# Kernel tuning notes

Hardware: AMD Instinct MI355X
Metric: run time of the kernel (lower is better)

Reference implementation:

```python
import jax, jax.numpy as jnp
import numpy as np

B, S, E, H = 4, 1024, 1024, 16
HD = E // H  # 64


def setup_inputs() -> dict:
    key = jax.random.key(0)
    ks = jax.random.split(key, 9)
    scale = 1.0 / np.sqrt(E)
    x = jax.random.normal(ks[0], (B, S, E), dtype=jnp.float32)
    attention_mask = jnp.ones((B, S, S), dtype=jnp.int32)
    # per-head projection weights, batched over heads: [H, E, HD]
    Wq = jax.random.normal(ks[1], (H, E, HD), dtype=jnp.float32) * scale
    Wk = jax.random.normal(ks[2], (H, E, HD), dtype=jnp.float32) * scale
    Wv = jax.random.normal(ks[3], (H, E, HD), dtype=jnp.float32) * scale
    bq = jax.random.normal(ks[4], (H, HD), dtype=jnp.float32) * scale
    bk = jax.random.normal(ks[5], (H, HD), dtype=jnp.float32) * scale
    bv = jax.random.normal(ks[6], (H, HD), dtype=jnp.float32) * scale
    # output projection, torch Linear convention: [out_features, in_features]
    Wo = jax.random.normal(ks[7], (E, E), dtype=jnp.float32) * scale
    bo = jax.random.normal(ks[8], (E,), dtype=jnp.float32) * scale
    return {"x": x, "attention_mask": attention_mask, "Wq": Wq, "bq": bq,
            "Wk": Wk, "bk": bk, "Wv": Wv, "bv": bv, "Wo": Wo, "bo": bo}


def reference(x, attention_mask, Wq, bq, Wk, bk, Wv, bv, Wo, bo):
    # batched-over-heads QKV projections: (B,S,E) x (H,E,HD) -> (B,H,S,HD)
    q = jnp.einsum('bse,hed->bhsd', x, Wq) + bq[None, :, None, :]
    k = jnp.einsum('bse,hed->bhsd', x, Wk) + bk[None, :, None, :]
    v = jnp.einsum('bse,hed->bhsd', x, Wv) + bv[None, :, None, :]
    scores = jnp.einsum('bhsd,bhtd->bhst', q, k) / jnp.sqrt(jnp.float32(HD))
    mask = attention_mask[:, None, :, :]  # (B,1,S,S) broadcast over heads
    scores = jnp.where(mask == 0, -jnp.inf, scores)
    weights = jax.nn.softmax(scores, axis=-1)
    out = jnp.einsum('bhst,bhtd->bhsd', weights, v)
    # concat heads on last dim: (B,S,H*HD) == (B,S,E)
    out = out.transpose(0, 2, 1, 3).reshape(B, S, E)
    return out @ Wo.T + bo
```

## Files before the change

### kernel.cpp

```cpp
#include <hip/hip_runtime.h>
#include <hip/hip_bf16.h>

#define NB 4
#define SEQ 1024
#define EMB 1024
#define NH 16
#define HD 64

typedef unsigned short u16;
typedef __attribute__((ext_vector_type(8))) __bf16 bf16x8;
typedef __attribute__((ext_vector_type(8))) short short8;
typedef __attribute__((ext_vector_type(4))) float floatx4;

__device__ inline u16 f2b_rn(float f) {
    union { float f; unsigned int i; } x; x.f = f;
    unsigned int r = (x.i + 0x7FFFu + ((x.i >> 16) & 1u)) >> 16;
    return (u16)r;
}
__device__ inline bf16x8 s2b(short8 v) {
    union { short8 s; bf16x8 b; } x; x.s = v; return x.b;
}

__device__ inline void gload_lds16(const void* g, void* l) {
    __builtin_amdgcn_global_load_lds(
        (const __attribute__((address_space(1))) void*)g,
        (__attribute__((address_space(3))) void*)l, 16, 0, 0);
}

__device__ inline bf16x8 ldsfrag(const u16* base, int r, int c) {
    return s2b(*(const short8*)&base[r * 64 + (c ^ ((r & 7) * 8))]);
}

__device__ inline void cvt8(const float* __restrict__ s, u16* __restrict__ d) {
    float4 a = *(const float4*)(s);
    float4 b = *(const float4*)(s + 4);
    union { u16 u[8]; int4 v; } o;
    o.u[0] = f2b_rn(a.x); o.u[1] = f2b_rn(a.y); o.u[2] = f2b_rn(a.z); o.u[3] = f2b_rn(a.w);
    o.u[4] = f2b_rn(b.x); o.u[5] = f2b_rn(b.y); o.u[6] = f2b_rn(b.z); o.u[7] = f2b_rn(b.w);
    *(int4*)(d) = o.v;
}

#define BARX do { __builtin_amdgcn_sched_barrier(0); __builtin_amdgcn_s_barrier(); __builtin_amdgcn_sched_barrier(0); } while(0)
#define VMCNT6 asm volatile("s_waitcnt vmcnt(6)" ::: "memory")
#define VMCNT5 asm volatile("s_waitcnt vmcnt(5)" ::: "memory")
#define VMCNT2 asm volatile("s_waitcnt vmcnt(2)" ::: "memory")
#define VMCNT0 asm volatile("s_waitcnt vmcnt(0)" ::: "memory")

__global__ __launch_bounds__(256) void prep(
    const float* __restrict__ x, const float* __restrict__ Wq,
    const float* __restrict__ Wk, const float* __restrict__ Wv,
    const int* __restrict__ mask,
    u16* __restrict__ xb, u16* __restrict__ Wt,
    unsigned long long* __restrict__ bits)
{
    __shared__ u16 T[64 * 80];
    int bx = blockIdx.x;
    int tid = threadIdx.x;

    if (bx < 512) {
        #pragma unroll
        for (int c = 0; c < 4; ++c) {
            int i = (bx * 4 + c) * 2048 + tid * 8;
            cvt8(x + i, xb + i);
        }
    } else if (bx < 1280) {
        int bx2 = bx - 512;
        int e0 = (bx2 & 15) * 64;
        int ph = bx2 >> 4;
        int p = ph >> 4, h = ph & 15;
        const float* W = (p == 0 ? Wq : (p == 1 ? Wk : Wv)) + h * (EMB * HD);
        #pragma unroll
        for (int c = 0; c < 2; ++c) {
            int flat = c * 2048 + tid * 8;
            int r = flat >> 6;
            int d = flat & 63;
            cvt8(W + (size_t)(e0 + r) * HD + d, &T[r * 80 + d]);
        }
        __syncthreads();
        int d = tid >> 2;
        int ec = tid & 3;
        union { u16 u[16]; int4 v[2]; } tmp;
        #pragma unroll
        for (int i = 0; i < 16; ++i) tmp.u[i] = T[(ec * 16 + i) * 80 + d];
        u16* dst = Wt + ((size_t)(p * NH + h) * HD + d) * EMB + e0 + ec * 16;
        *(int4*)(dst) = tmp.v[0];
        *(int4*)(dst + 8) = tmp.v[1];
    } else {
        int base = (bx - 1280) * 16 + (tid >> 6) * 4;
        int lane = tid & 63;
        #pragma unroll
        for (int i = 0; i < 4; ++i) {
            int gw = base + i;
            int m = mask[(size_t)gw * 64 + lane];
            unsigned long long bl = __ballot(m != 0);
            if (lane == 0) bits[gw] = bl;
        }
    }
}

__device__ __forceinline__ void rd_b(const u16* B, int wn, int ln, int quad, bf16x8 (&bfr)[4][2]) {
    #pragma unroll
    for (int nc = 0; nc < 4; ++nc) {
        bfr[nc][0] = ldsfrag(B, wn * 64 + nc * 16 + ln, quad * 8);
        bfr[nc][1] = ldsfrag(B, wn * 64 + nc * 16 + ln, 32 + quad * 8);
    }
}
__device__ __forceinline__ void rd_a(const u16* A, int wm, int mf0, int ln, int quad, bf16x8 (&a)[2][2]) {
    #pragma unroll
    for (int jj = 0; jj < 2; ++jj) {
        a[jj][0] = ldsfrag(A, wm * 128 + (mf0 + jj) * 16 + ln, quad * 8);
        a[jj][1] = ldsfrag(A, wm * 128 + (mf0 + jj) * 16 + ln, 32 + quad * 8);
    }
}
__device__ __forceinline__ void mm8(floatx4 (&acc)[8][4], const bf16x8 (&a)[2][2],
                                    const bf16x8 (&bfr)[4][2], int mf0) {
    #pragma unroll
    for (int jj = 0; jj < 2; ++jj)
        #pragma unroll
        for (int nc = 0; nc < 4; ++nc) {
            acc[mf0 + jj][nc] = __builtin_amdgcn_mfma_f32_16x16x32_bf16(a[jj][0], bfr[nc][0], acc[mf0 + jj][nc], 0, 0, 0);
            acc[mf0 + jj][nc] = __builtin_amdgcn_mfma_f32_16x16x32_bf16(a[jj][1], bfr[nc][1], acc[mf0 + jj][nc], 0, 0, 0);
        }
}

#define STG(srcb, buf, c, kt) gload_lds16((srcb) + (size_t)(c) * 65536 + (kt) * 64 + soff, (buf) + (c) * 4096 + ldst)

__global__ __launch_bounds__(512, 2) void qkv_gemm(
    const u16* __restrict__ x,
    const u16* __restrict__ Wt2,
    const float* __restrict__ bq, const float* __restrict__ bk, const float* __restrict__ bv,
    u16* __restrict__ Q, u16* __restrict__ K, u16* __restrict__ Vt)
{
    __shared__ u16 L[65536];
    u16* A0s = L;
    u16* A1s = L + 16384;
    u16* B0s = L + 32768;
    u16* B1s = L + 49152;

    int gid = blockIdx.x;
    int xcd = gid & 7;
    int j   = gid >> 3;
    int mt_ = (xcd >> 1) * 4 + (j & 3);
    int nt_ = (xcd & 1) * 6 + (j >> 2);
    int m0 = mt_ * 256;
    int n0 = nt_ * 256;

    int tid = threadIdx.x;
    int w = tid >> 6, lane = tid & 63, quad = lane >> 4, ln = lane & 15;
    int wm = w >> 2, wn = w & 3;

    const u16* Asrc = x   + (size_t)m0 * EMB;
    const u16* Bsrc = Wt2 + (size_t)n0 * EMB;

    int sr = tid >> 3;
    int sc = ((tid & 7) ^ (sr & 7)) * 8;
    size_t soff = (size_t)sr * EMB + sc;
    int ldst = w * 512;

    STG(Asrc, A0s, 0, 0); STG(Asrc, A0s, 1, 0); STG(Asrc, A0s, 2, 0); STG(Asrc, A0s, 3, 0);
    STG(Bsrc, B0s, 0, 0); STG(Bsrc, B0s, 1, 0); STG(Bsrc, B0s, 2, 0); STG(Bsrc, B0s, 3, 0);
    STG(Bsrc, B1s, 0, 1); STG(Bsrc, B1s, 1, 1); STG(Bsrc, B1s, 2, 1); STG(Bsrc, B1s, 3, 1);
    STG(Asrc, A1s, 0, 1); STG(Asrc, A1s, 2, 1);
    VMCNT6;
    BARX;

    floatx4 acc[8][4] = {};
    bf16x8 bfr[4][2];
    bf16x8 a[2][2];

    for (int i = 0; i < 8; ++i) {
        const int T = 2 * i;
        const bool st = (i < 7);
        rd_b(B0s, wn, ln, quad, bfr);
        rd_a(A0s, wm, 0, ln, quad, a);
        STG(Asrc, A1s, 1, T + 1); STG(Asrc, A1s, 3, T + 1);
        BARX;
        __builtin_amdgcn_s_setprio(1); mm8(acc, a, bfr, 0); __builtin_amdgcn_s_setprio(0);
        BARX;
        rd_a(A0s, wm, 2, ln, quad, a);
        if (st) { STG(Bsrc, B0s, 0, T + 2); STG(Bsrc, B0s, 1, T + 2); }
        BARX;
        __builtin_amdgcn_s_setprio(1); mm8(acc, a, bfr, 2); __builtin_amdgcn_s_setprio(0);
        BARX;
        rd_a(A0s, wm, 4, ln, quad, a);
        if (st) { STG(Bsrc, B0s, 2, T + 2); STG(Bsrc, B0s, 3, T + 2); }
        BARX;
        __builtin_amdgcn_s_setprio(1); mm8(acc, a, bfr, 4); __builtin_amdgcn_s_setprio(0);
        BARX;
        rd_a(A0s, wm, 6, ln, quad, a);
        if (st) { STG(Asrc, A0s, 0, T + 2); STG(Asrc, A0s, 2, T + 2); }
        BARX;
        __builtin_amdgcn_s_setprio(1); mm8(acc, a, bfr, 6); __builtin_amdgcn_s_setprio(0);
        if (st) { VMCNT6; } else { VMCNT0; }
        BARX;
        rd_b(B1s, wn, ln, quad, bfr);
        rd_a(A1s, wm, 0, ln, quad, a);
        if (st) { STG(Asrc, A0s, 1, T + 2); STG(Asrc, A0s, 3, T + 2); }
        BARX;
        __builtin_amdgcn_s_setprio(1); mm8(acc, a, bfr, 0); __builtin_amdgcn_s_setprio(0);
        BARX;
        rd_a(A1s, wm, 2, ln, quad, a);
        if (st) { STG(Bsrc, B1s, 0, T + 3); STG(Bsrc, B1s, 1, T + 3); }
        BARX;
        __builtin_amdgcn_s_setprio(1); mm8(acc, a, bfr, 2); __builtin_amdgcn_s_setprio(0);
        BARX;
        rd_a(A1s, wm, 4, ln, quad, a);
        if (st) { STG(Bsrc, B1s, 2, T + 3); STG(Bsrc, B1s, 3, T + 3); }
        BARX;
        __builtin_amdgcn_s_setprio(1); mm8(acc, a, bfr, 4); __builtin_amdgcn_s_setprio(0);
        BARX;
        rd_a(A1s, wm, 6, ln, quad, a);
        if (st) { STG(Asrc, A1s, 0, T + 3); STG(Asrc, A1s, 2, T + 3); }
        BARX;
        __builtin_amdgcn_s_setprio(1); mm8(acc, a, bfr, 6); __builtin_amdgcn_s_setprio(0);
        if (st) { VMCNT6; }
        BARX;
    }

    int nbase = n0 + wn * 64;
    int p = nbase >> 10;
    int h = (nbase >> 6) & 15;
    const float* bias = (p == 0 ? bq : (p == 1 ? bk : bv));
    if (p < 2) {
        u16* Out = (p == 0) ? Q : K;
        float qs = (p == 0) ? 0.125f * 1.44269504f : 1.0f;
        #pragma unroll
        for (int nc = 0; nc < 4; ++nc) {
            int d = nc * 16 + ln;
            float bv_ = bias[(nbase & 1023) + d];
            #pragma unroll
            for (int mf = 0; mf < 8; ++mf) {
                #pragma unroll
                for (int reg = 0; reg < 4; ++reg) {
                    int m = m0 + wm * 128 + mf * 16 + quad * 4 + reg;
                    int b_ = m >> 10, s = m & 1023;
                    Out[((size_t)(b_ * NH + h) * SEQ + s) * HD + d] = f2b_rn((acc[mf][nc][reg] + bv_) * qs);
                }
            }
        }
    } else {
        #pragma unroll
        for (int nc = 0; nc < 4; ++nc) {
            int d = nc * 16 + ln;
            float bv_ = bias[(nbase & 1023) + d];
            #pragma unroll
            for (int mf = 0; mf < 8; ++mf) {
                int m = m0 + wm * 128 + mf * 16 + quad * 4;
                int b_ = m >> 10, s = m & 1023;
                union { u16 u[4]; uint2 v; } pk;
                #pragma unroll
                for (int reg = 0; reg < 4; ++reg)
                    pk.u[reg] = f2b_rn(acc[mf][nc][reg] + bv_);
                *(uint2*)&Vt[((size_t)(b_ * NH + h) * HD + d) * SEQ + s] = pk.v;
            }
        }
    }
}

__device__ __forceinline__ void astage(const u16* __restrict__ Kb, const u16* __restrict__ Vb,
                                       u16* Kd, u16* Vd, int t0, int tid) {
    #pragma unroll
    for (int i = 0; i < 2; ++i) {
        int flat0 = i * 256 + (tid & 192);
        int flat = flat0 + (tid & 63);
        int r = flat >> 3;
        int c = ((flat & 7) ^ (r & 7)) * 8;
        gload_lds16(Kb + (size_t)(t0 + r) * HD + c, Kd + flat0 * 8);
        gload_lds16(Vb + (size_t)r * SEQ + t0 + c, Vd + flat0 * 8);
    }
}

__device__ __forceinline__ void attn_tile(
    const u16* Ksc, const u16* Vsc, u16* Ps,
    const bf16x8 (&qf)[2][2], floatx4 (&o)[2][5],
    unsigned long long bm0, unsigned long long bm1,
    int w, int ln, int quad)
{
    const int PP = 72;
    floatx4 sc[2][4] = {};
    #pragma unroll
    for (int kk = 0; kk < 2; ++kk) {
        bf16x8 kf[4];
        #pragma unroll
        for (int tb = 0; tb < 4; ++tb)
            kf[tb] = ldsfrag(Ksc, tb * 16 + ln, kk * 32 + quad * 8);
        __builtin_amdgcn_s_setprio(1);
        #pragma unroll
        for (int s = 0; s < 2; ++s)
            #pragma unroll
            for (int tb = 0; tb < 4; ++tb)
                sc[s][tb] = __builtin_amdgcn_mfma_f32_16x16x32_bf16(kf[tb], qf[s][kk], sc[s][tb], 0, 0, 0);
        __builtin_amdgcn_s_setprio(0);
    }

    #pragma unroll
    for (int s = 0; s < 2; ++s) {
        unsigned long long bm = s ? bm1 : bm0;
        if (__any(bm != ~0ull)) {
            #pragma unroll
            for (int tb = 0; tb < 4; ++tb)
                #pragma unroll
                for (int reg = 0; reg < 4; ++reg)
                    if (!((bm >> (tb * 16 + quad * 4 + reg)) & 1)) sc[s][tb][reg] = -1e30f;
        }
    }

    #pragma unroll
    for (int s = 0; s < 2; ++s) {
        int mrow = w * 32 + s * 16 + ln;
        #pragma unroll
        for (int tb = 0; tb < 4; ++tb) {
            union { float f; unsigned int i; } e0_, e1_, e2_, e3_;
            e0_.f = __builtin_amdgcn_exp2f(sc[s][tb][0]);
            e1_.f = __builtin_amdgcn_exp2f(sc[s][tb][1]);
            e2_.f = __builtin_amdgcn_exp2f(sc[s][tb][2]);
            e3_.f = __builtin_amdgcn_exp2f(sc[s][tb][3]);
            uint2 pk;
            pk.x = ((e0_.i + 0x8000u) >> 16) | ((e1_.i + 0x8000u) & 0xFFFF0000u);
            pk.y = ((e2_.i + 0x8000u) >> 16) | ((e3_.i + 0x8000u) & 0xFFFF0000u);
            *(uint2*)&Ps[mrow * PP + tb * 16 + quad * 4] = pk;
        }
    }

    #pragma unroll
    for (int kk = 0; kk < 2; ++kk) {
        bf16x8 vf[5];
        #pragma unroll
        for (int dt = 0; dt < 5; ++dt)
            vf[dt] = ldsfrag(Vsc, dt * 16 + ln, kk * 32 + quad * 8);
        #pragma unroll
        for (int s = 0; s < 2; ++s) {
            bf16x8 pf = s2b(*(const short8*)&Ps[(w * 32 + s * 16 + ln) * PP + kk * 32 + quad * 8]);
            __builtin_amdgcn_s_setprio(1);
            #pragma unroll
            for (int dt = 0; dt < 5; ++dt)
                o[s][dt] = __builtin_amdgcn_mfma_f32_16x16x32_bf16(pf, vf[dt], o[s][dt], 0, 0, 0);
            __builtin_amdgcn_s_setprio(0);
        }
    }
}

__global__ __launch_bounds__(256) void attn(
    const u16* __restrict__ Q, const u16* __restrict__ K, const u16* __restrict__ Vt,
    const unsigned long long* __restrict__ bits,
    const float* __restrict__ Wo, u16* __restrict__ Wob,
    u16* __restrict__ Aout)
{
    __shared__ u16 L[16512 + 128 * 72];
    u16* Ks0 = L;
    u16* Ks1 = L + 4096;
    u16* Vs0 = L + 8192;
    u16* Vs1 = L + 12352;
    u16* Ps  = L + 16512;

    int bid = blockIdx.x;
    int tid = threadIdx.x;

    if (bid >= 512) {
        int i = (bid - 512) * 2048 + tid * 8;
        cvt8(Wo + i, Wob + i);
        return;
    }

    int bh = bid & 63;
    int q0 = (bid >> 6) * 128;
    int b = bh >> 4, h = bh & 15;
    const u16* Qb = Q  + (size_t)bh * SEQ * HD;
    const u16* Kb = K  + (size_t)bh * SEQ * HD;
    const u16* Vb = Vt + (size_t)bh * HD * SEQ;

    int w = tid >> 6, lane = tid & 63, quad = lane >> 4, ln = lane & 15;

    if (tid < 32) {
        u16* dst = (tid < 16 ? L + 12288 : L + 16448) + (tid & 15) * 4;
        *(uint2*)dst = make_uint2(0x3F803F80u, 0x3F803F80u);
    }

    bf16x8 qf[2][2];
    #pragma unroll
    for (int s = 0; s < 2; ++s) {
        const u16* qp = Qb + (size_t)(q0 + w * 32 + s * 16 + ln) * HD + quad * 8;
        union { int4 i; bf16x8 b; } c0, c1;
        c0.i = *(const int4*)(qp);
        c1.i = *(const int4*)(qp + 32);
        qf[s][0] = c0.b; qf[s][1] = c1.b;
    }

    __syncthreads();

    astage(Kb, Vb, Ks0, Vs0, 0,  tid);
    astage(Kb, Vb, Ks1, Vs1, 64, tid);
    size_t bb0 = ((size_t)b * SEQ + q0 + w * 32 + ln) * 16;
    size_t bb1 = bb0 + 256;
    unsigned long long bmn0 = bits[bb0];
    unsigned long long bmn1 = bits[bb1];

    floatx4 o[2][5] = {};

    for (int i = 0; i < 8; ++i) {
        VMCNT6;
        BARX;
        {
            unsigned long long bc0 = bmn0, bc1 = bmn1;
            bmn0 = bits[bb0 + (2 * i + 1)];
            bmn1 = bits[bb1 + (2 * i + 1)];
            attn_tile(Ks0, Vs0, Ps, qf, o, bc0, bc1, w, ln, quad);
        }
        BARX;
        if (i < 7) astage(Kb, Vb, Ks0, Vs0, i * 128 + 128, tid);
        if (i < 7) { VMCNT6; } else { VMCNT2; }
        BARX;
        {
            unsigned long long bc0 = bmn0, bc1 = bmn1;
            if (i < 7) { bmn0 = bits[bb0 + (2 * i + 2)]; bmn1 = bits[bb1 + (2 * i + 2)]; }
            attn_tile(Ks1, Vs1, Ps, qf, o, bc0, bc1, w, ln, quad);
        }
        BARX;
        if (i < 7) astage(Kb, Vb, Ks1, Vs1, i * 128 + 192, tid);
    }

    #pragma unroll
    for (int s = 0; s < 2; ++s) {
        #pragma unroll
        for (int reg = 0; reg < 4; ++reg) {
            float l = __shfl(o[s][4][reg], lane & 48, 64);
            float inv = 1.0f / l;
            int m = q0 + w * 32 + s * 16 + quad * 4 + reg;
            #pragma unroll
            for (int dt = 0; dt < 4; ++dt)
                Aout[((size_t)b * SEQ + m) * EMB + h * HD + dt * 16 + ln] = f2b_rn(o[s][dt][reg] * inv);
        }
    }
}

#define OSTG_A(buf, kt) gload_lds16(Asrc + (size_t)(kt) * 64 + soff, (buf) + ldst)
#define OSTG_B(buf, c, kt) gload_lds16(Bsrc + (size_t)(c) * 65536 + (size_t)(kt) * 64 + soff, (buf) + (c) * 4096 + ldst)

__device__ __forceinline__ void op_tile(const u16* As, const u16* Bs,
                                        floatx4 (&acc)[4][2], int w, int ln, int quad)
{
    #pragma unroll
    for (int kk = 0; kk < 2; ++kk) {
        bf16x8 av[4], bv2[2];
        #pragma unroll
        for (int mf = 0; mf < 4; ++mf)
            av[mf] = ldsfrag(As, mf * 16 + ln, kk * 32 + quad * 8);
        #pragma unroll
        for (int nc = 0; nc < 2; ++nc)
            bv2[nc] = ldsfrag(Bs, w * 32 + nc * 16 + ln, kk * 32 + quad * 8);
        __builtin_amdgcn_s_setprio(1);
        #pragma unroll
        for (int mf = 0; mf < 4; ++mf)
            #pragma unroll
            for (int nc = 0; nc < 2; ++nc)
                acc[mf][nc] = __builtin_amdgcn_mfma_f32_16x16x32_bf16(av[mf], bv2[nc], acc[mf][nc], 0, 0, 0);
        __builtin_amdgcn_s_setprio(0);
    }
}

__global__ __launch_bounds__(512, 2) void out_proj(
    const u16* __restrict__ A,
    const u16* __restrict__ Wo,
    const float* __restrict__ bo,
    float* __restrict__ Out)
{
    __shared__ u16 L[40960];
    u16* A0s = L;
    u16* A1s = L + 4096;
    u16* B0s = L + 8192;
    u16* B1s = L + 24576;

    int gid = blockIdx.x;
    int xcd = gid & 7;
    int j   = gid >> 3;
    int m0 = (xcd * 8 + (j & 7)) * 64;
    int n0 = (j >> 3) * 256;

    int tid = threadIdx.x;
    int w = tid >> 6, lane = tid & 63, quad = lane >> 4, ln = lane & 15;

    const u16* Asrc = A  + (size_t)m0 * EMB;
    const u16* Bsrc = Wo + (size_t)n0 * EMB;
    int sr = tid >> 3;
    int sc = ((tid & 7) ^ (sr & 7)) * 8;
    size_t soff = (size_t)sr * EMB + sc;
    int ldst = w * 512;

    OSTG_A(A0s, 0); OSTG_B(B0s, 0, 0); OSTG_B(B0s, 1, 0); OSTG_B(B0s, 2, 0); OSTG_B(B0s, 3, 0);
    OSTG_A(A1s, 1); OSTG_B(B1s, 0, 1); OSTG_B(B1s, 1, 1); OSTG_B(B1s, 2, 1); OSTG_B(B1s, 3, 1);

    floatx4 acc[4][2] = {};

    for (int i = 0; i < 8; ++i) {
        VMCNT5;
        BARX;
        op_tile(A0s, B0s, acc, w, ln, quad);
        BARX;
        if (i < 7) {
            int kt = 2 * i + 2;
            OSTG_A(A0s, kt); OSTG_B(B0s, 0, kt); OSTG_B(B0s, 1, kt); OSTG_B(B0s, 2, kt); OSTG_B(B0s, 3, kt);
        }
        if (i < 7) { VMCNT5; } else { VMCNT0; }
        BARX;
        op_tile(A1s, B1s, acc, w, ln, quad);
        BARX;
        if (i < 7) {
            int kt = 2 * i + 3;
            OSTG_A(A1s, kt); OSTG_B(B1s, 0, kt); OSTG_B(B1s, 1, kt); OSTG_B(B1s, 2, kt); OSTG_B(B1s, 3, kt);
        }
    }

    #pragma unroll
    for (int nc = 0; nc < 2; ++nc) {
        int n = n0 + w * 32 + nc * 16 + ln;
        float bb = bo[n];
        #pragma unroll
        for (int mf = 0; mf < 4; ++mf) {
            #pragma unroll
            for (int reg = 0; reg < 4; ++reg) {
                int m = m0 + mf * 16 + quad * 4 + reg;
                Out[(size_t)m * EMB + n] = acc[mf][nc][reg] + bb;
            }
        }
    }
}

extern "C" void kernel_launch(void* const* d_in, const int* in_sizes, int n_in,
                              void* d_out, int out_size, void* d_ws, size_t ws_size,
                              hipStream_t stream) {
    const float* x  = (const float*)d_in[0];
    const int*   mk = (const int*)d_in[1];
    const float* Wq = (const float*)d_in[2];
    const float* bq = (const float*)d_in[3];
    const float* Wk = (const float*)d_in[4];
    const float* bk = (const float*)d_in[5];
    const float* Wv = (const float*)d_in[6];
    const float* bv = (const float*)d_in[7];
    const float* Wo = (const float*)d_in[8];
    const float* bo = (const float*)d_in[9];
    float* out = (float*)d_out;

    const size_t MB = 1u << 20;
    char* ws = (char*)d_ws;
    u16* xb  = (u16*)ws;
    u16* Wt  = (u16*)(ws + 8 * MB);
    u16* Wob = (u16*)(ws + 14 * MB);
    unsigned long long* bits = (unsigned long long*)(ws + 16 * MB);
    u16* Qw  = (u16*)(ws + 16 * MB + 512 * 1024);
    u16* Kw  = (u16*)(ws + 24 * MB + 512 * 1024);
    u16* Vtw = (u16*)(ws + 32 * MB + 512 * 1024);
    u16* Ao  = xb;

    prep<<<5376, 256, 0, stream>>>(x, Wq, Wk, Wv, mk, xb, Wt, bits);
    qkv_gemm<<<192, 512, 0, stream>>>(xb, Wt, bq, bk, bv, Qw, Kw, Vtw);
    attn<<<1024, 256, 0, stream>>>(Qw, Kw, Vtw, bits, Wo, Wob, Ao);
    out_proj<<<256, 512, 0, stream>>>(Ao, Wob, bo, out);
}
```

Before: 183.9 us.

## Shrink QKV GEMM N-tile to 192 so grid fills all 256 CUs

Changes the QKV projection GEMM tile from 256x256 to 256x192, which raises the grid from 192 to 256 blocks so every CU on the MI355X gets work. The B stage shrinks to three chunks, the staging schedule and vmcnt waits are rebalanced, and the epilogue now resolves projection and head per 16-column fragment because a 192-wide tile can straddle heads and Q/K/V. The aim is to remove the wave quantization that left CUs idle. The cost is lower arithmetic intensity per block and a more complex epilogue.

```diff
diff --git a/kernel.cpp b/kernel.cpp
--- a/kernel.cpp
+++ b/kernel.cpp
@@ -98,11 +98,11 @@
     }
 }
 
-__device__ __forceinline__ void rd_b(const u16* B, int wn, int ln, int quad, bf16x8 (&bfr)[4][2]) {
-    #pragma unroll
-    for (int nc = 0; nc < 4; ++nc) {
-        bfr[nc][0] = ldsfrag(B, wn * 64 + nc * 16 + ln, quad * 8);
-        bfr[nc][1] = ldsfrag(B, wn * 64 + nc * 16 + ln, 32 + quad * 8);
+__device__ __forceinline__ void rd_b3(const u16* B, int wn, int ln, int quad, bf16x8 (&bfr)[3][2]) {
+    #pragma unroll
+    for (int nc = 0; nc < 3; ++nc) {
+        bfr[nc][0] = ldsfrag(B, wn * 48 + nc * 16 + ln, quad * 8);
+        bfr[nc][1] = ldsfrag(B, wn * 48 + nc * 16 + ln, 32 + quad * 8);
     }
 }
 __device__ __forceinline__ void rd_a(const u16* A, int wm, int mf0, int ln, int quad, bf16x8 (&a)[2][2]) {
@@ -112,12 +112,12 @@
         a[jj][1] = ldsfrag(A, wm * 128 + (mf0 + jj) * 16 + ln, 32 + quad * 8);
     }
 }
-__device__ __forceinline__ void mm8(floatx4 (&acc)[8][4], const bf16x8 (&a)[2][2],
-                                    const bf16x8 (&bfr)[4][2], int mf0) {
+__device__ __forceinline__ void mm12(floatx4 (&acc)[8][3], const bf16x8 (&a)[2][2],
+                                     const bf16x8 (&bfr)[3][2], int mf0) {
     #pragma unroll
     for (int jj = 0; jj < 2; ++jj)
         #pragma unroll
-        for (int nc = 0; nc < 4; ++nc) {
+        for (int nc = 0; nc < 3; ++nc) {
             acc[mf0 + jj][nc] = __builtin_amdgcn_mfma_f32_16x16x32_bf16(a[jj][0], bfr[nc][0], acc[mf0 + jj][nc], 0, 0, 0);
             acc[mf0 + jj][nc] = __builtin_amdgcn_mfma_f32_16x16x32_bf16(a[jj][1], bfr[nc][1], acc[mf0 + jj][nc], 0, 0, 0);
         }
@@ -131,19 +131,19 @@
     const float* __restrict__ bq, const float* __restrict__ bk, const float* __restrict__ bv,
     u16* __restrict__ Q, u16* __restrict__ K, u16* __restrict__ Vt)
 {
-    __shared__ u16 L[65536];
+    __shared__ u16 L[57344];
     u16* A0s = L;
     u16* A1s = L + 16384;
     u16* B0s = L + 32768;
-    u16* B1s = L + 49152;
+    u16* B1s = L + 45056;
 
     int gid = blockIdx.x;
     int xcd = gid & 7;
     int j   = gid >> 3;
     int mt_ = (xcd >> 1) * 4 + (j & 3);
-    int nt_ = (xcd & 1) * 6 + (j >> 2);
+    int nt_ = (xcd & 1) * 8 + (j >> 2);
     int m0 = mt_ * 256;
-    int n0 = nt_ * 256;
+    int n0 = nt_ * 192;
 
     int tid = threadIdx.x;
     int w = tid >> 6, lane = tid & 63, quad = lane >> 4, ln = lane & 15;
@@ -158,76 +158,77 @@
     int ldst = w * 512;
 
     STG(Asrc, A0s, 0, 0); STG(Asrc, A0s, 1, 0); STG(Asrc, A0s, 2, 0); STG(Asrc, A0s, 3, 0);
-    STG(Bsrc, B0s, 0, 0); STG(Bsrc, B0s, 1, 0); STG(Bsrc, B0s, 2, 0); STG(Bsrc, B0s, 3, 0);
-    STG(Bsrc, B1s, 0, 1); STG(Bsrc, B1s, 1, 1); STG(Bsrc, B1s, 2, 1); STG(Bsrc, B1s, 3, 1);
+    STG(Bsrc, B0s, 0, 0); STG(Bsrc, B0s, 1, 0); STG(Bsrc, B0s, 2, 0);
+    STG(Bsrc, B1s, 0, 1); STG(Bsrc, B1s, 1, 1); STG(Bsrc, B1s, 2, 1);
     STG(Asrc, A1s, 0, 1); STG(Asrc, A1s, 2, 1);
-    VMCNT6;
+    VMCNT5;
     BARX;
 
-    floatx4 acc[8][4] = {};
-    bf16x8 bfr[4][2];
+    floatx4 acc[8][3] = {};
+    bf16x8 bfr[3][2];
     bf16x8 a[2][2];
 
     for (int i = 0; i < 8; ++i) {
         const int T = 2 * i;
         const bool st = (i < 7);
-        rd_b(B0s, wn, ln, quad, bfr);
+        rd_b3(B0s, wn, ln, quad, bfr);
         rd_a(A0s, wm, 0, ln, quad, a);
         STG(Asrc, A1s, 1, T + 1); STG(Asrc, A1s, 3, T + 1);
         BARX;
-        __builtin_amdgcn_s_setprio(1); mm8(acc, a, bfr, 0); __builtin_amdgcn_s_setprio(0);
+        __builtin_amdgcn_s_setprio(1); mm12(acc, a, bfr, 0); __builtin_amdgcn_s_setprio(0);
         BARX;
         rd_a(A0s, wm, 2, ln, quad, a);
         if (st) { STG(Bsrc, B0s, 0, T + 2); STG(Bsrc, B0s, 1, T + 2); }
         BARX;
-        __builtin_amdgcn_s_setprio(1); mm8(acc, a, bfr, 2); __builtin_amdgcn_s_setprio(0);
+        __builtin_amdgcn_s_setprio(1); mm12(acc, a, bfr, 2); __builtin_amdgcn_s_setprio(0);
         BARX;
         rd_a(A0s, wm, 4, ln, quad, a);
-        if (st) { STG(Bsrc, B0s, 2, T + 2); STG(Bsrc, B0s, 3, T + 2); }
-        BARX;
-        __builtin_amdgcn_s_setprio(1); mm8(acc, a, bfr, 4); __builtin_amdgcn_s_setprio(0);
+        if (st) { STG(Bsrc, B0s, 2, T + 2); STG(Asrc, A0s, 0, T + 2); }
+        BARX;
+        __builtin_amdgcn_s_setprio(1); mm12(acc, a, bfr, 4); __builtin_amdgcn_s_setprio(0);
         BARX;
         rd_a(A0s, wm, 6, ln, quad, a);
-        if (st) { STG(Asrc, A0s, 0, T + 2); STG(Asrc, A0s, 2, T + 2); }
-        BARX;
-        __builtin_amdgcn_s_setprio(1); mm8(acc, a, bfr, 6); __builtin_amdgcn_s_setprio(0);
-        if (st) { VMCNT6; } else { VMCNT0; }
-        BARX;
-        rd_b(B1s, wn, ln, quad, bfr);
+        if (st) { STG(Asrc, A0s, 2, T + 2); }
+        BARX;
+        __builtin_amdgcn_s_setprio(1); mm12(acc, a, bfr, 6); __builtin_amdgcn_s_setprio(0);
+        if (st) { VMCNT5; } else { VMCNT0; }
+        BARX;
+        rd_b3(B1s, wn, ln, quad, bfr);
         rd_a(A1s, wm, 0, ln, quad, a);
         if (st) { STG(Asrc, A0s, 1, T + 2); STG(Asrc, A0s, 3, T + 2); }
         BARX;
-        __builtin_amdgcn_s_setprio(1); mm8(acc, a, bfr, 0); __builtin_amdgcn_s_setprio(0);
+        __builtin_amdgcn_s_setprio(1); mm12(acc, a, bfr, 0); __builtin_amdgcn_s_setprio(0);
         BARX;
         rd_a(A1s, wm, 2, ln, quad, a);
         if (st) { STG(Bsrc, B1s, 0, T + 3); STG(Bsrc, B1s, 1, T + 3); }
         BARX;
-        __builtin_amdgcn_s_setprio(1); mm8(acc, a, bfr, 2); __builtin_amdgcn_s_setprio(0);
+        __builtin_amdgcn_s_setprio(1); mm12(acc, a, bfr, 2); __builtin_amdgcn_s_setprio(0);
         BARX;
         rd_a(A1s, wm, 4, ln, quad, a);
-        if (st) { STG(Bsrc, B1s, 2, T + 3); STG(Bsrc, B1s, 3, T + 3); }
-        BARX;
-        __builtin_amdgcn_s_setprio(1); mm8(acc, a, bfr, 4); __builtin_amdgcn_s_setprio(0);
+        if (st) { STG(Bsrc, B1s, 2, T + 3); STG(Asrc, A1s, 0, T + 3); }
+        BARX;
+        __builtin_amdgcn_s_setprio(1); mm12(acc, a, bfr, 4); __builtin_amdgcn_s_setprio(0);
         BARX;
         rd_a(A1s, wm, 6, ln, quad, a);
-        if (st) { STG(Asrc, A1s, 0, T + 3); STG(Asrc, A1s, 2, T + 3); }
-        BARX;
-        __builtin_amdgcn_s_setprio(1); mm8(acc, a, bfr, 6); __builtin_amdgcn_s_setprio(0);
-        if (st) { VMCNT6; }
-        BARX;
-    }
-
-    int nbase = n0 + wn * 64;
-    int p = nbase >> 10;
-    int h = (nbase >> 6) & 15;
-    const float* bias = (p == 0 ? bq : (p == 1 ? bk : bv));
-    if (p < 2) {
-        u16* Out = (p == 0) ? Q : K;
-        float qs = (p == 0) ? 0.125f * 1.44269504f : 1.0f;
-        #pragma unroll
-        for (int nc = 0; nc < 4; ++nc) {
-            int d = nc * 16 + ln;
-            float bv_ = bias[(nbase & 1023) + d];
+        if (st) { STG(Asrc, A1s, 2, T + 3); }
+        BARX;
+        __builtin_amdgcn_s_setprio(1); mm12(acc, a, bfr, 6); __builtin_amdgcn_s_setprio(0);
+        if (st) { VMCNT5; }
+        BARX;
+    }
+
+    int nb_w = n0 + wn * 48;
+    #pragma unroll
+    for (int nc = 0; nc < 3; ++nc) {
+        int nbc = nb_w + nc * 16;
+        int p = nbc >> 10;
+        int h = (nbc >> 6) & 15;
+        const float* bias = (p == 0 ? bq : (p == 1 ? bk : bv));
+        int d = (nbc & 63) + ln;
+        float bv_ = bias[(nbc & 1023) + ln];
+        if (p < 2) {
+            u16* Out = (p == 0) ? Q : K;
+            float qs = (p == 0) ? 0.125f * 1.44269504f : 1.0f;
             #pragma unroll
             for (int mf = 0; mf < 8; ++mf) {
                 #pragma unroll
@@ -237,12 +238,7 @@
                     Out[((size_t)(b_ * NH + h) * SEQ + s) * HD + d] = f2b_rn((acc[mf][nc][reg] + bv_) * qs);
                 }
             }
-        }
-    } else {
-        #pragma unroll
-        for (int nc = 0; nc < 4; ++nc) {
-            int d = nc * 16 + ln;
-            float bv_ = bias[(nbase & 1023) + d];
+        } else {
             #pragma unroll
             for (int mf = 0; mf < 8; ++mf) {
                 int m = m0 + wm * 128 + mf * 16 + quad * 4;
@@ -552,7 +548,7 @@
     u16* Ao  = xb;
 
     prep<<<5376, 256, 0, stream>>>(x, Wq, Wk, Wv, mk, xb, Wt, bits);
-    qkv_gemm<<<192, 512, 0, stream>>>(xb, Wt, bq, bk, bv, Qw, Kw, Vtw);
+    qkv_gemm<<<256, 512, 0, stream>>>(xb, Wt, bq, bk, bv, Qw, Kw, Vtw);
     attn<<<1024, 256, 0, stream>>>(Qw, Kw, Vtw, bits, Wo, Wob, Ao);
     out_proj<<<256, 512, 0, stream>>>(Ao, Wob, bo, out);
 }
```

After: 177.8 us. -3.3%, faster.
